# Kernel tuning notes

Hardware: AMD Instinct MI355X
Metric: run time of the kernel (lower is better)

The kernel has to match this reference:

```python
import jax, jax.numpy as jnp
from jax import lax
import numpy as np

B, C, H, W = 8, 256, 64, 64
DSTATE, DCONV, EXPAND = 16, 4, 2
DI = EXPAND * C          # 512 d_inner
DTR = (C + 15) // 16     # 16 dt_rank = ceil(d_model/16)

# ---------- helpers ----------

def _ln(x, g, b):
    m = x.mean(-1, keepdims=True)
    v = x.var(-1, keepdims=True)
    return (x - m) * lax.rsqrt(v + 1e-5) * g + b


def _bn(x, g, b):  # BatchNorm2d, training-mode batch stats
    m = x.mean((0, 2, 3), keepdims=True)
    v = x.var((0, 2, 3), keepdims=True)
    return (x - m) * lax.rsqrt(v + 1e-5) * g[None, :, None, None] + b[None, :, None, None]


def _gn(x, g, b, groups=32):
    Bb, Cc, Hh, Ww = x.shape
    xr = x.reshape(Bb, groups, Cc // groups, Hh, Ww)
    m = xr.mean((2, 3, 4), keepdims=True)
    v = xr.var((2, 3, 4), keepdims=True)
    xr = (xr - m) * lax.rsqrt(v + 1e-5)
    return xr.reshape(Bb, Cc, Hh, Ww) * g[None, :, None, None] + b[None, :, None, None]


def _hsig(x):  # h_sigmoid: relu6(x+3)/6
    return jnp.clip(x + 3.0, 0.0, 6.0) / 6.0


def _axial(v, idx, pos):
    # v: [B,C,N]; pos: [1,C,16] linearly resized to N (align_corners=False == half-pixel)
    N = v.shape[-1]
    pe = jax.image.resize(pos, (1, pos.shape[1], N), method='linear')
    return v + pe + idx  # idx interpolation is identity (same size)


def _dwconvT(x, w):
    # ConvTranspose2d(k=3, stride=2, pad=1, out_pad=1, groups=C) == lhs-dilated corr with flipped kernel
    wf = w[:, :, ::-1, ::-1]
    return lax.conv_general_dilated(x, wf, window_strides=(1, 1), padding=((1, 2), (1, 2)),
                                    lhs_dilation=(2, 2), dimension_numbers=('NCHW', 'OIHW', 'NCHW'),
                                    feature_group_count=x.shape[1])


def _mamba(h, in_w, conv_w, conv_b, xproj_w, dt_w, dt_b, Alog, Dp, out_w):
    # standard mamba_ssm Mamba block forward; h: [B,L,d_model]
    Bb, L, _ = h.shape
    di = in_w.shape[0] // 2
    N = Alog.shape[1]
    dtr = dt_w.shape[1]
    xz = h @ in_w.T                      # [B,L,2*di]
    xm, zg = xz[..., :di], xz[..., di:]
    # causal depthwise conv1d (pad K-1 left == torch pad both + slice [:L])
    xc = lax.conv_general_dilated(xm.transpose(0, 2, 1), conv_w, (1,), [(conv_w.shape[2] - 1, 0)],
                                  dimension_numbers=('NCH', 'OIH', 'NCH'), feature_group_count=di)
    u = jax.nn.silu(xc + conv_b[None, :, None]).transpose(0, 2, 1)  # [B,L,di]
    dbl = u @ xproj_w.T                  # [B,L,dtr+2N]
    dt = jax.nn.softplus(dbl[..., :dtr] @ dt_w.T + dt_b)            # [B,L,di]
    Bm = dbl[..., dtr:dtr + N]
    Cm = dbl[..., dtr + N:]
    A = -jnp.exp(Alog)                   # [di,N]
    dA = jnp.exp(dt[..., None] * A)      # [B,L,di,N]
    dBu = (dt * u)[..., None] * Bm[:, :, None, :]

    def step(hst, inp):
        dA_t, dBu_t = inp
        hst = dA_t * hst + dBu_t
        return hst, hst

    h0 = jnp.zeros((Bb, di, N), dt.dtype)
    _, hs = lax.scan(step, h0, (dA.transpose(1, 0, 2, 3), dBu.transpose(1, 0, 2, 3)))
    y = jnp.einsum('lbdn,bln->bld', hs, Cm) + Dp * u
    y = y * jax.nn.silu(zg)
    return y @ out_w.T


def _forward(x, pos_embed, ln_w, ln_b, proj_w, proj_b,
             up_dw_w, up_bn1_g, up_bn1_b, up_pw_w, up_bn2_g, up_bn2_b,
             down_pw_w, down_bn_g, down_bn_b, gn_g, gn_b,
             f_in_w, f_conv_w, f_conv_b, f_xproj_w, f_dt_w, f_dt_b, f_Alog, f_D, f_out_w,
             b_in_w, b_conv_w, b_conv_b, b_xproj_w, b_dt_w, b_dt_b, b_Alog, b_D, b_out_w):
    # upsample branch: dwconvT -> BN -> ReLU -> 1x1 -> BN -> ReLU6
    z = _dwconvT(x, up_dw_w)
    z = jax.nn.relu(_bn(z, up_bn1_g, up_bn1_b))
    z = jnp.einsum('oc,bchw->bohw', up_pw_w, z)
    z = jnp.clip(_bn(z, up_bn2_g, up_bn2_b), 0.0, 6.0)  # act1 = ReLU6
    dt = x.dtype
    col_max = _ln(_axial(x.max(2), jnp.argmax(x, 2).astype(dt), pos_embed).transpose(0, 2, 1), ln_w, ln_b)
    col_min = _ln(_axial(x.min(2), jnp.argmin(x, 2).astype(dt), pos_embed).transpose(0, 2, 1), ln_w, ln_b)
    row_max = _ln(_axial(x.max(3), jnp.argmax(x, 3).astype(dt), pos_embed).transpose(0, 2, 1), ln_w, ln_b)
    row_min = _ln(_axial(x.min(3), jnp.argmin(x, 3).astype(dt), pos_embed).transpose(0, 2, 1), ln_w, ln_b)
    result_max = jnp.concatenate([col_max, row_max], 1)  # [B, W+H, C]
    result_min = jnp.concatenate([col_min, row_min], 1)
    fpar = (f_in_w, f_conv_w, f_conv_b, f_xproj_w, f_dt_w, f_dt_b, f_Alog, f_D, f_out_w)
    bpar = (b_in_w, b_conv_w, b_conv_b, b_xproj_w, b_dt_w, b_dt_b, b_Alog, b_D, b_out_w)
    fmax = _ln(_mamba(result_max, *fpar), ln_w, ln_b)
    fmin = _ln(_mamba(result_min, *fpar), ln_w, ln_b)
    bmax = _ln(_mamba(jnp.flip(result_max, 1), *bpar), ln_w, ln_b)
    bmin = _ln(_mamba(jnp.flip(result_min, 1), *bpar), ln_w, ln_b)
    res_max = jnp.concatenate([fmax, jnp.flip(bmax, 1)], -1) @ proj_w.T + proj_b
    res_max = _ln(res_max, ln_w, ln_b)
    res_min = jnp.concatenate([fmin, jnp.flip(bmin, 1)], -1) @ proj_w.T + proj_b
    res_min = _ln(res_min, ln_w, ln_b)
    res = res_max[:, :, None, :] + res_min[:, None, :, :]  # [B,L,L,C], L=H+W
    res = res.transpose(0, 3, 1, 2)                        # [B,C,L,L] == [B,C,2H,2W]
    res = _hsig(res) * z
    res = _gn(res, gn_g, gn_b)
    res = jnp.einsum('oc,bchw->bohw', down_pw_w, res[:, :, ::2, ::2])  # 1x1 stride-2 conv
    res = _bn(res, down_bn_g, down_bn_b)
    res = _gn(res, gn_g, gn_b)
    res = res + x
    res = _gn(res, gn_g, gn_b)
    return res


def setup_inputs() -> dict:
    key = jax.random.key(0)
    ks = jax.random.split(key, 32)

    def n(i, shape, s=0.02):
        return jax.random.normal(ks[i], shape, jnp.float32) * s

    inp = {}
    inp['x'] = jax.random.normal(ks[0], (B, C, H, W), jnp.float32)
    inp['pos_embed'] = jax.random.normal(ks[1], (1, C, 16), jnp.float32)
    inp['ln_w'] = jnp.ones((C,), jnp.float32)
    inp['ln_b'] = jnp.zeros((C,), jnp.float32)
    inp['proj_w'] = n(2, (C, 2 * C))
    inp['proj_b'] = jnp.zeros((C,), jnp.float32)
    inp['up_dw_w'] = n(3, (C, 1, 3, 3), 0.1)
    inp['up_bn1_g'] = jnp.ones((C,), jnp.float32)
    inp['up_bn1_b'] = jnp.zeros((C,), jnp.float32)
    inp['up_pw_w'] = n(4, (C, C), 0.05)
    inp['up_bn2_g'] = jnp.ones((C,), jnp.float32)
    inp['up_bn2_b'] = jnp.zeros((C,), jnp.float32)
    inp['down_pw_w'] = n(5, (C, C), 0.05)
    inp['down_bn_g'] = jnp.ones((C,), jnp.float32)
    inp['down_bn_b'] = jnp.zeros((C,), jnp.float32)
    inp['gn_g'] = jnp.ones((C,), jnp.float32)
    inp['gn_b'] = jnp.zeros((C,), jnp.float32)
    Alog = jnp.tile(jnp.log(jnp.arange(1, DSTATE + 1, dtype=jnp.float32))[None, :], (DI, 1))
    dtb = jnp.full((DI,), float(np.log(np.expm1(0.01))), jnp.float32)
    for p, k0 in (('f', 6), ('b', 16)):
        inp[p + '_in_w'] = n(k0, (2 * DI, C))
        inp[p + '_conv_w'] = n(k0 + 1, (DI, 1, DCONV), 0.2)
        inp[p + '_conv_b'] = jnp.zeros((DI,), jnp.float32)
        inp[p + '_xproj_w'] = n(k0 + 2, (DTR + 2 * DSTATE, DI))
        inp[p + '_dt_w'] = n(k0 + 3, (DI, DTR), 0.1)
        inp[p + '_dt_b'] = dtb
        inp[p + '_Alog'] = Alog
        inp[p + '_D'] = jnp.ones((DI,), jnp.float32)
        inp[p + '_out_w'] = n(k0 + 4, (C, DI))
    return inp


def reference(x, pos_embed, ln_w, ln_b, proj_w, proj_b,
              up_dw_w, up_bn1_g, up_bn1_b, up_pw_w, up_bn2_g, up_bn2_b,
              down_pw_w, down_bn_g, down_bn_b, gn_g, gn_b,
              f_in_w, f_conv_w, f_conv_b, f_xproj_w, f_dt_w, f_dt_b, f_Alog, f_D, f_out_w,
              b_in_w, b_conv_w, b_conv_b, b_xproj_w, b_dt_w, b_dt_b, b_Alog, b_D, b_out_w):
    return _forward(x, pos_embed, ln_w, ln_b, proj_w, proj_b,
                    up_dw_w, up_bn1_g, up_bn1_b, up_pw_w, up_bn2_g, up_bn2_b,
                    down_pw_w, down_bn_g, down_bn_b, gn_g, gn_b,
                    f_in_w, f_conv_w, f_conv_b, f_xproj_w, f_dt_w, f_dt_b, f_Alog, f_D, f_out_w,
                    b_in_w, b_conv_w, b_conv_b, b_xproj_w, b_dt_w, b_dt_b, b_Alog, b_D, b_out_w)
```

## Files before the change

### kernel.cpp

```cpp
#include <hip/hip_runtime.h>
#include <hip/hip_bf16.h>

typedef __hip_bfloat16 bf16;
typedef __attribute__((ext_vector_type(8))) short bf16x8v;
typedef __attribute__((ext_vector_type(4))) short bf16x4v;
typedef __attribute__((ext_vector_type(4))) float f32x4v;

#define B_ 8
#define C_ 256
#define L_ 128
#define MB 1048576UL

__device__ inline float b2f(bf16 v){ return __bfloat162float(v); }
__device__ inline bf16 f2b(float v){ return __float2bfloat16(v); }
__device__ inline short b2s(bf16 v){ return *(short*)&v; }
__device__ inline float siluf(float x){ return x / (1.f + expf(-x)); }
__device__ inline float softplusf(float x){ return (x > 20.f) ? x : log1pf(expf(x)); }
__device__ inline float vclamp(float v){ return fmaxf(v, 0.f) + 1e-5f; }

__device__ inline void bred2(float& a, float& b, float* red){
  #pragma unroll
  for (int m = 1; m < 64; m <<= 1){ a += __shfl_xor(a, m); b += __shfl_xor(b, m); }
  int tid = threadIdx.x, wave = tid >> 6, lane = tid & 63;
  __syncthreads();
  if (lane == 0){ red[wave] = a; red[8 + wave] = b; }
  __syncthreads();
  a = red[0] + red[1] + red[2] + red[3];
  b = red[8] + red[9] + red[10] + red[11];
}

__device__ inline int tswz(int p, int c){
  return (p*512 + c*2) ^ (((p ^ (p >> 2)) & 7) << 4);
}

__global__ __launch_bounds__(64) void pool1_kernel(const float* __restrict__ x, const float* __restrict__ pos,
    float* __restrict__ pcolmax, float* __restrict__ pcolmin,
    float* __restrict__ prowmax, float* __restrict__ prowmin, float* __restrict__ sxb)
{
  int c = blockIdx.x, b = blockIdx.y, t = threadIdx.x;
  __shared__ float xs[64][65];
  const float* xp = x + ((long)(b*C_ + c))*4096;
  const float4* xp4 = (const float4*)xp;
  #pragma unroll
  for (int q = 0; q < 16; q++){
    float4 v = xp4[q*64 + t];
    int e = q*64 + t;
    int i = e >> 4, cc = (e & 15) << 2;
    xs[i][cc] = v.x; xs[i][cc+1] = v.y; xs[i][cc+2] = v.z; xs[i][cc+3] = v.w;
  }
  __syncthreads();
  float tt = 0.25f*(float)t - 0.375f;
  const float* pp = pos + c*16;
  float pe;
  if (tt <= 0.f) pe = pp[0];
  else if (tt >= 15.f) pe = pp[15];
  else { int f = (int)floorf(tt); float w = tt - (float)f; pe = pp[f]*(1.f - w) + pp[f+1]*w; }
  float vmax = -1e30f, vmin = 1e30f; int amax = 0, amin = 0;
  for (int j = 0; j < 64; j++){
    float v = xs[t][j];
    if (v > vmax){ vmax = v; amax = j; }
    if (v < vmin){ vmin = v; amin = j; }
  }
  long o = (long)(b*64 + t)*C_ + c;
  prowmax[o] = vmax + pe + (float)amax;
  prowmin[o] = vmin + pe + (float)amin;
  vmax = -1e30f; vmin = 1e30f; amax = 0; amin = 0;
  float sx = 0.f, sx2 = 0.f;
  for (int i = 0; i < 64; i++){
    float v = xs[i][t];
    if (v > vmax){ vmax = v; amax = i; }
    if (v < vmin){ vmin = v; amin = i; }
    sx += v; sx2 += v*v;
  }
  pcolmax[o] = vmax + pe + (float)amax;
  pcolmin[o] = vmin + pe + (float)amin;
  #pragma unroll
  for (int m = 1; m < 64; m <<= 1){ sx += __shfl_xor(sx, m); sx2 += __shfl_xor(sx2, m); }
  if (t == 0){ sxb[(b << 8) + c] = sx; sxb[2048 + (b << 8) + c] = sx2; }
}

__global__ __launch_bounds__(256) void pool2_kernel(const float* __restrict__ pcolmax, const float* __restrict__ pcolmin,
    const float* __restrict__ prowmax, const float* __restrict__ prowmin,
    const float* __restrict__ lnw, const float* __restrict__ lnb, bf16* __restrict__ hbuf)
{
  int r = blockIdx.x, b = blockIdx.y, c = threadIdx.x;
  __shared__ float red[16];
  int p = r & 63;
  long src = (long)(b*64 + p)*C_ + c;
  float vmax = (r < 64) ? pcolmax[src] : prowmax[src];
  float vmin = (r < 64) ? pcolmin[src] : prowmin[src];
  float gw = lnw[c], gb = lnb[c];
  long row = (long)b*L_ + r, frow = (long)b*L_ + (127 - r);
  float s = vmax, s2 = vmax*vmax;
  bred2(s, s2, red);
  float m = s*(1.f/256.f), var = s2*(1.f/256.f) - m*m;
  float o = (vmax - m)*rsqrtf(vclamp(var))*gw + gb;
  hbuf[0*262144 + row*C_ + c]  = f2b(o);
  hbuf[2*262144 + frow*C_ + c] = f2b(o);
  s = vmin; s2 = vmin*vmin;
  bred2(s, s2, red);
  m = s*(1.f/256.f); var = s2*(1.f/256.f) - m*m;
  o = (vmin - m)*rsqrtf(vclamp(var))*gw + gb;
  hbuf[1*262144 + row*C_ + c]  = f2b(o);
  hbuf[3*262144 + frow*C_ + c] = f2b(o);
}

__global__ __launch_bounds__(256) void dwz1_kernel(const float* __restrict__ x, const float* __restrict__ dw,
    bf16* __restrict__ z1, float* __restrict__ bn1sum, float* __restrict__ bn1sq)
{
  int bc = blockIdx.x; int c = bc & 255;
  int tid = threadIdx.x;
  __shared__ __align__(16) float xs[4096];
  const float4* xp4 = (const float4*)(x + (long)bc*4096);
  #pragma unroll
  for (int q = 0; q < 4; q++)
    *(float4*)&xs[(q*256 + tid)*4] = xp4[q*256 + tid];
  float w[9];
  #pragma unroll
  for (int q = 0; q < 9; q++) w[q] = dw[c*9 + q];
  __syncthreads();
  bf16* zp = z1 + (long)bc*16384;
  float s = 0.f, s2 = 0.f;
  for (int it = 0; it < 64; it++){
    int p = it*256 + tid; int i = p >> 7, j = p & 127;
    int xi = i >> 1, xj = j >> 1;
    int io = i & 1, jo = j & 1;
    int xi1 = (xi < 63) ? xi + 1 : 63;
    int xj1 = (xj < 63) ? xj + 1 : 63;
    float XA = xs[xi*64 + xj];
    float XB = xs[xi*64 + xj1];
    float XC = xs[xi1*64 + xj];
    float XD = xs[xi1*64 + xj1];
    float wA = jo ? (io ? w[8] : w[5]) : (io ? w[7] : w[4]);
    float wB = (jo && j < 127) ? (io ? w[6] : w[3]) : 0.f;
    float wC = (io && i < 127) ? (jo ? w[2] : w[1]) : 0.f;
    float wD = (io && jo && i < 127 && j < 127) ? w[0] : 0.f;
    float acc = wA*XA;
    acc += wB*XB;
    acc += wC*XC;
    acc += wD*XD;
    zp[p] = f2b(acc);
    s += acc; s2 += acc*acc;
  }
  __shared__ float red[16];
  bred2(s, s2, red);
  if (tid == 0){ atomicAdd(&bn1sum[c], s); atomicAdd(&bn1sq[c], s2); }
}

__global__ __launch_bounds__(256) void wcvt_all_kernel(
    const float* __restrict__ s0, const float* __restrict__ s1, const float* __restrict__ s2,
    const float* __restrict__ s3, const float* __restrict__ s4, const float* __restrict__ s5,
    const float* __restrict__ s6, const float* __restrict__ s7, const float* __restrict__ s8,
    bf16* __restrict__ d0, bf16* __restrict__ d1, bf16* __restrict__ d2,
    bf16* __restrict__ d3, bf16* __restrict__ d4, bf16* __restrict__ d5,
    bf16* __restrict__ d6, bf16* __restrict__ d7, bf16* __restrict__ d8)
{
  int seg = blockIdx.y;
  const float* s; bf16* d; int n;
  switch (seg){
    case 0: s = s0; d = d0; n = 262144; break;
    case 1: s = s1; d = d1; n = 262144; break;
    case 2: s = s2; d = d2; n = 24576;  break;
    case 3: s = s3; d = d3; n = 24576;  break;
    case 4: s = s4; d = d4; n = 131072; break;
    case 5: s = s5; d = d5; n = 131072; break;
    case 6: s = s6; d = d6; n = 131072; break;
    case 7: s = s7; d = d7; n = 65536;  break;
    default: s = s8; d = d8; n = 65536; break;
  }
  long i = ((long)blockIdx.x*256 + threadIdx.x)*4;
  if (i >= n) return;
  float4 v = *(const float4*)&s[i];
  bf16 o[4] = {f2b(v.x), f2b(v.y), f2b(v.z), f2b(v.w)};
  *(uint2*)&d[i] = *(const uint2*)o;
}

__global__ __launch_bounds__(256) void pwz_fused_kernel(const bf16* __restrict__ z1,
    const float* __restrict__ bn1sum, const float* __restrict__ bn1sq,
    const float* __restrict__ g1, const float* __restrict__ b1,
    const bf16* __restrict__ Wb, bf16* __restrict__ z2,
    float* __restrict__ bn2part)
{
  int b = blockIdx.y;
  int p0 = blockIdx.x*64;
  int tid = threadIdx.x;
  __shared__ __align__(16) short Tb[16384];
  __shared__ float aa[256], dd[256];
  {
    float m = bn1sum[tid]*(1.f/131072.f);
    float v = bn1sq[tid]*(1.f/131072.f) - m*m;
    float a = g1[tid]*rsqrtf(vclamp(v));
    aa[tid] = a; dd[tid] = b1[tid] - m*a;
  }
  __syncthreads();
  {
    int pc = tid & 15, ch = tid >> 4;
    #pragma unroll
    for (int it = 0; it < 8; it++){
      int c = (ch + it*16)*2;
      const bf16* r0 = &z1[((long)(b*C_ + c))*16384 + p0 + pc*4];
      bf16x4v va = *(const bf16x4v*)r0;
      bf16x4v vb = *(const bf16x4v*)(r0 + 16384);
      float a0 = aa[c], d0 = dd[c], a1 = aa[c+1], d1 = dd[c+1];
      #pragma unroll
      for (int k = 0; k < 4; k++){
        int p = pc*4 + k;
        bf16 h0; *(short*)&h0 = va[k];
        bf16 h1; *(short*)&h1 = vb[k];
        bf16 o0 = f2b(fmaxf(b2f(h0)*a0 + d0, 0.f));
        bf16 o1 = f2b(fmaxf(b2f(h1)*a1 + d1, 0.f));
        unsigned int u = ((unsigned int)(*(unsigned short*)&o1) << 16) | (unsigned int)(*(unsigned short*)&o0);
        *(unsigned int*)((char*)Tb + tswz(p, c)) = u;
      }
    }
  }
  __syncthreads();
  int wave = tid >> 6, lane = tid & 63;
  int quad = lane >> 4, l16 = lane & 15;
  f32x4v acc[4][4];
  #pragma unroll
  for (int i = 0; i < 4; i++)
    #pragma unroll
    for (int j = 0; j < 4; j++) acc[i][j] = (f32x4v){0.f, 0.f, 0.f, 0.f};
  for (int k0 = 0; k0 < 256; k0 += 32){
    int c = k0 + quad*8;
    bf16x8v a[4], bb[4];
    #pragma unroll
    for (int ms = 0; ms < 4; ms++)
      a[ms] = *(const bf16x8v*)&Wb[(wave*64 + ms*16 + l16)*C_ + c];
    #pragma unroll
    for (int ns = 0; ns < 4; ns++){
      int p = ns*16 + l16;
      bb[ns] = *(const bf16x8v*)((const char*)Tb + tswz(p, c));
    }
    #pragma unroll
    for (int ms = 0; ms < 4; ms++)
      #pragma unroll
      for (int ns = 0; ns < 4; ns++)
        acc[ms][ns] = __builtin_amdgcn_mfma_f32_16x16x32_bf16(bb[ns], a[ms], acc[ms][ns], 0, 0, 0);
  }
  int slot = (blockIdx.x & 7) | (b << 3);
  #pragma unroll
  for (int ms = 0; ms < 4; ms++){
    int o = wave*64 + ms*16 + l16;
    long rowbase = ((long)(b*C_ + o))*16384 + p0;
    float s = 0.f, s2 = 0.f;
    #pragma unroll
    for (int ns = 0; ns < 4; ns++){
      bf16 ov[4];
      #pragma unroll
      for (int r = 0; r < 4; r++){
        bf16 bv = f2b(acc[ms][ns][r]);
        ov[r] = bv;
        float vv = b2f(bv);
        s += vv; s2 += vv*vv;
      }
      *(uint2*)&z2[rowbase + ns*16 + quad*4] = *(const uint2*)ov;
    }
    s += __shfl_xor(s, 16);  s += __shfl_xor(s, 32);
    s2 += __shfl_xor(s2, 16); s2 += __shfl_xor(s2, 32);
    if (quad == 0){
      atomicAdd(&bn2part[slot*256 + o], s);
      atomicAdd(&bn2part[16384 + slot*256 + o], s2);
    }
  }
}

__global__ __launch_bounds__(256) void inproj_mfma_kernel(const bf16* __restrict__ hb,
    const bf16* __restrict__ Wif, const bf16* __restrict__ Wib2, bf16* __restrict__ xz)
{
  int v = blockIdx.z;
  int m0 = blockIdx.y*256, n0 = blockIdx.x*64;
  const bf16* A = hb + (long)v*262144;
  const bf16* W = (v >= 2) ? Wib2 : Wif;
  bf16* out = xz + (long)v*1048576;
  int tid = threadIdx.x;
  int wave = tid >> 6, lane = tid & 63;
  int quad = lane >> 4, l16 = lane & 15;
  f32x4v acc[4][4];
  #pragma unroll
  for (int i = 0; i < 4; i++)
    #pragma unroll
    for (int j = 0; j < 4; j++) acc[i][j] = (f32x4v){0.f, 0.f, 0.f, 0.f};
  for (int k0 = 0; k0 < 256; k0 += 32){
    int c = k0 + quad*8;
    bf16x8v a[4], bb[4];
    #pragma unroll
    for (int ms = 0; ms < 4; ms++)
      a[ms] = *(const bf16x8v*)&A[(long)(m0 + wave*64 + ms*16 + l16)*256 + c];
    #pragma unroll
    for (int ns = 0; ns < 4; ns++)
      bb[ns] = *(const bf16x8v*)&W[(long)(n0 + ns*16 + l16)*256 + c];
    #pragma unroll
    for (int ms = 0; ms < 4; ms++)
      #pragma unroll
      for (int ns = 0; ns < 4; ns++)
        acc[ms][ns] = __builtin_amdgcn_mfma_f32_16x16x32_bf16(bb[ns], a[ms], acc[ms][ns], 0, 0, 0);
  }
  #pragma unroll
  for (int ms = 0; ms < 4; ms++){
    int m = m0 + wave*64 + ms*16 + l16;
    #pragma unroll
    for (int ns = 0; ns < 4; ns++){
      bf16 ov[4];
      #pragma unroll
      for (int r = 0; r < 4; r++) ov[r] = f2b(acc[ms][ns][r]);
      *(uint2*)&out[(long)m*1024 + n0 + ns*16 + quad*4] = *(const uint2*)ov;
    }
  }
}

__global__ __launch_bounds__(256) void xproj_mfma_kernel(const bf16* __restrict__ ub,
    const bf16* __restrict__ Wxf, const bf16* __restrict__ Wxb, float* __restrict__ dblb)
{
  int v = blockIdx.y;
  int m0 = blockIdx.x*256;
  const bf16* A = ub + (long)v*524288;
  const bf16* W = (v >= 2) ? Wxb : Wxf;
  float* out = dblb + (long)v*49152;
  int tid = threadIdx.x;
  int wave = tid >> 6, lane = tid & 63;
  int quad = lane >> 4, l16 = lane & 15;
  f32x4v acc[4][3];
  #pragma unroll
  for (int i = 0; i < 4; i++)
    #pragma unroll
    for (int j = 0; j < 3; j++) acc[i][j] = (f32x4v){0.f, 0.f, 0.f, 0.f};
  for (int k0 = 0; k0 < 512; k0 += 32){
    int c = k0 + quad*8;
    bf16x8v a[4], bb[3];
    #pragma unroll
    for (int ms = 0; ms < 4; ms++)
      a[ms] = *(const bf16x8v*)&A[(long)(m0 + wave*64 + ms*16 + l16)*512 + c];
    #pragma unroll
    for (int ns = 0; ns < 3; ns++)
      bb[ns] = *(const bf16x8v*)&W[(long)(ns*16 + l16)*512 + c];
    #pragma unroll
    for (int ms = 0; ms < 4; ms++)
      #pragma unroll
      for (int ns = 0; ns < 3; ns++)
        acc[ms][ns] = __builtin_amdgcn_mfma_f32_16x16x32_bf16(bb[ns], a[ms], acc[ms][ns], 0, 0, 0);
  }
  #pragma unroll
  for (int ms = 0; ms < 4; ms++){
    int m = m0 + wave*64 + ms*16 + l16;
    #pragma unroll
    for (int ns = 0; ns < 3; ns++)
      *(f32x4v*)&out[(long)m*48 + ns*16 + quad*4] = acc[ms][ns];
  }
}

__global__ __launch_bounds__(256) void outproj_mfma_kernel(const bf16* __restrict__ yb,
    const bf16* __restrict__ Wof, const bf16* __restrict__ Wob, float* __restrict__ mo)
{
  int v = blockIdx.z;
  int m0 = blockIdx.y*256, n0 = blockIdx.x*64;
  const bf16* A = yb + (long)v*524288;
  const bf16* W = (v >= 2) ? Wob : Wof;
  float* out = mo + (long)v*262144;
  int tid = threadIdx.x;
  int wave = tid >> 6, lane = tid & 63;
  int quad = lane >> 4, l16 = lane & 15;
  f32x4v acc[4][4];
  #pragma unroll
  for (int i = 0; i < 4; i++)
    #pragma unroll
    for (int j = 0; j < 4; j++) acc[i][j] = (f32x4v){0.f, 0.f, 0.f, 0.f};
  for (int k0 = 0; k0 < 512; k0 += 32){
    int c = k0 + quad*8;
    bf16x8v a[4], bb[4];
    #pragma unroll
    for (int ms = 0; ms < 4; ms++)
      a[ms] = *(const bf16x8v*)&A[(long)(m0 + wave*64 + ms*16 + l16)*512 + c];
    #pragma unroll
    for (int ns = 0; ns < 4; ns++)
      bb[ns] = *(const bf16x8v*)&W[(long)(n0 + ns*16 + l16)*512 + c];
    #pragma unroll
    for (int ms = 0; ms < 4; ms++)
      #pragma unroll
      for (int ns = 0; ns < 4; ns++)
        acc[ms][ns] = __builtin_amdgcn_mfma_f32_16x16x32_bf16(bb[ns], a[ms], acc[ms][ns], 0, 0, 0);
  }
  #pragma unroll
  for (int ms = 0; ms < 4; ms++){
    int m = m0 + wave*64 + ms*16 + l16;
    #pragma unroll
    for (int ns = 0; ns < 4; ns++)
      *(f32x4v*)&out[(long)m*256 + n0 + ns*16 + quad*4] = acc[ms][ns];
  }
}

__global__ __launch_bounds__(256) void pj_mfma_kernel(const bf16* __restrict__ cb,
    const bf16* __restrict__ Wp, const float* __restrict__ pb, float* __restrict__ rp)
{
  int z = blockIdx.z;
  int m0 = blockIdx.y*256, n0 = blockIdx.x*64;
  const bf16* A = cb + (long)z*524288;
  float* out = rp + (long)z*262144;
  int tid = threadIdx.x;
  int wave = tid >> 6, lane = tid & 63;
  int quad = lane >> 4, l16 = lane & 15;
  f32x4v acc[4][4];
  #pragma unroll
  for (int i = 0; i < 4; i++)
    #pragma unroll
    for (int j = 0; j < 4; j++) acc[i][j] = (f32x4v){0.f, 0.f, 0.f, 0.f};
  for (int k0 = 0; k0 < 512; k0 += 32){
    int c = k0 + quad*8;
    bf16x8v a[4], bb[4];
    #pragma unroll
    for (int ms = 0; ms < 4; ms++)
      a[ms] = *(const bf16x8v*)&A[(long)(m0 + wave*64 + ms*16 + l16)*512 + c];
    #pragma unroll
    for (int ns = 0; ns < 4; ns++)
      bb[ns] = *(const bf16x8v*)&Wp[(long)(n0 + ns*16 + l16)*512 + c];
    #pragma unroll
    for (int ms = 0; ms < 4; ms++)
      #pragma unroll
      for (int ns = 0; ns < 4; ns++)
        acc[ms][ns] = __builtin_amdgcn_mfma_f32_16x16x32_bf16(bb[ns], a[ms], acc[ms][ns], 0, 0, 0);
  }
  #pragma unroll
  for (int ns = 0; ns < 4; ns++){
    float4 pbv = *(const float4*)&pb[n0 + ns*16 + quad*4];
    #pragma unroll
    for (int ms = 0; ms < 4; ms++){
      int m = m0 + wave*64 + ms*16 + l16;
      f32x4v vv = acc[ms][ns];
      vv[0] += pbv.x; vv[1] += pbv.y; vv[2] += pbv.z; vv[3] += pbv.w;
      *(f32x4v*)&out[(long)m*256 + n0 + ns*16 + quad*4] = vv;
    }
  }
}

__global__ __launch_bounds__(256) void gemm_kernel(
  const float* __restrict__ Abase, long sA, int lda,
  const float* __restrict__ W0, const float* __restrict__ W1,
  const float* __restrict__ bias0, const float* __restrict__ bias1, int wsplit,
  float* __restrict__ Cbase, long sC, int ldc,
  int M, int N, int K, int act)
{
  int z = blockIdx.z;
  const float* A = Abase + (long)z*sA;
  const float* W = (z >= wsplit) ? W1 : W0;
  const float* bias = (z >= wsplit) ? bias1 : bias0;
  int m0 = blockIdx.y*64, n0 = blockIdx.x*64;
  __shared__ __align__(16) float As[16][68];
  __shared__ __align__(16) float Ws[16][68];
  int tid = threadIdx.x, tx = tid & 15, ty = tid >> 4;
  float acc[4][4] = {};
  for (int k0 = 0; k0 < K; k0 += 16){
    #pragma unroll
    for (int q = 0; q < 4; q++){
      int e = tid + q*256; int r = e >> 4, kk = e & 15;
      int mi = m0 + r, ki = k0 + kk;
      As[kk][r] = (mi < M && ki < K) ? A[(long)mi*lda + ki] : 0.f;
    }
    #pragma unroll
    for (int q = 0; q < 4; q++){
      int e = tid + q*256; int n = e >> 4, kk = e & 15;
      int ni = n0 + n, ki = k0 + kk;
      Ws[kk][n] = (ni < N && ki < K) ? W[(long)ni*K + ki] : 0.f;
    }
    __syncthreads();
    #pragma unroll
    for (int kk = 0; kk < 16; kk++){
      float4 a4 = *(const float4*)&As[kk][ty*4];
      float4 b4 = *(const float4*)&Ws[kk][tx*4];
      float av[4] = {a4.x, a4.y, a4.z, a4.w};
      float bv[4] = {b4.x, b4.y, b4.z, b4.w};
      #pragma unroll
      for (int mm = 0; mm < 4; mm++)
        #pragma unroll
        for (int nn = 0; nn < 4; nn++) acc[mm][nn] += av[mm]*bv[nn];
    }
    __syncthreads();
  }
  #pragma unroll
  for (int mm = 0; mm < 4; mm++){
    int mi = m0 + ty*4 + mm;
    if (mi >= M) continue;
    #pragma unroll
    for (int nn = 0; nn < 4; nn++){
      int ni = n0 + tx*4 + nn;
      if (ni >= N) continue;
      float v = acc[mm][nn];
      if (bias) v += bias[ni];
      if (act >= 2) v = softplusf(v);
      if (act == 3){
        bf16* Cb = (bf16*)Cbase + (long)z*sC;
        Cb[(long)mi*ldc + ni] = f2b(v);
      } else {
        float* Cp = Cbase + (long)z*sC;
        Cp[(long)mi*ldc + ni] = v;
      }
    }
  }
}

__global__ __launch_bounds__(512) void conv1d_kernel(const bf16* __restrict__ xzb,
    const float* __restrict__ fw, const float* __restrict__ fb,
    const float* __restrict__ bw, const float* __restrict__ bb,
    bf16* __restrict__ ub)
{
  int l = blockIdx.x, b = blockIdx.y, v = blockIdx.z, d = threadIdx.x;
  const bf16* xm = xzb + (long)v*1024*1024;
  const float* w  = (v < 2) ? fw : bw;
  const float* cb = (v < 2) ? fb : bb;
  float acc = cb[d];
  #pragma unroll
  for (int k = 0; k < 4; k++){
    int ll = l - 3 + k;
    if (ll >= 0) acc += b2f(xm[(long)(b*L_ + ll)*1024 + d]) * w[d*4 + k];
  }
  ub[(long)v*1024*512 + (long)(b*L_ + l)*512 + d] = f2b(siluf(acc));
}

__global__ __launch_bounds__(64) void scan_kernel(const bf16* __restrict__ dtb, const bf16* __restrict__ ub,
    const float* __restrict__ dblb, const bf16* __restrict__ xzb,
    const float* __restrict__ fAlog, const float* __restrict__ fD,
    const float* __restrict__ bAlog, const float* __restrict__ bD,
    bf16* __restrict__ yb)
{
  int v = blockIdx.z, b = blockIdx.y;
  int tid = threadIdx.x;
  int dd = tid & 15, qtr = tid >> 4;
  int d0 = blockIdx.x*16;
  int d = d0 + dd;
  const bf16*  dt  = dtb  + (long)v*1024*512;
  const bf16*  u   = ub   + (long)v*1024*512;
  const float* dbl = dblb + (long)v*1024*48;
  const bf16*  zg  = xzb  + (long)v*1024*1024 + 512;
  const float* Alog = (v < 2) ? fAlog : bAlog;
  const float* Dp   = (v < 2) ? fD : bD;
  __shared__ __align__(16) short sdt[16][136];
  __shared__ __align__(16) short su_[16][136];
  __shared__ __align__(16) short szg[16][136];
  __shared__ __align__(16) short sB [16][136];
  __shared__ __align__(16) short sC [16][136];
  long row = (long)b*L_;
  for (int idx = tid; idx < 2048; idx += 64){
    int l = idx >> 4, j = idx & 15;
    sdt[j][l] = b2s(dt[(row + l)*512 + d0 + j]);
    su_[j][l] = b2s(u[(row + l)*512 + d0 + j]);
    szg[j][l] = b2s(zg[(row + l)*1024 + d0 + j]);
    sB [j][l] = b2s(f2b(dbl[(row + l)*48 + 16 + j]));
    sC [j][l] = b2s(f2b(dbl[(row + l)*48 + 32 + j]));
  }
  float a2[4];
  #pragma unroll
  for (int n = 0; n < 4; n++) a2[n] = -expf(Alog[d*16 + qtr*4 + n]) * 1.44269504f;
  float Dv = Dp[d];
  float h[4];
  #pragma unroll
  for (int n = 0; n < 4; n++) h[n] = 0.f;
  __syncthreads();
  bf16* yo = yb + (long)v*1024*512;
  for (int l0 = 0; l0 < 128; l0 += 8){
    bf16x8v dt8 = *(const bf16x8v*)&sdt[dd][l0];
    bf16x8v u8  = *(const bf16x8v*)&su_[dd][l0];
    bf16x8v zg8 = *(const bf16x8v*)&szg[dd][l0];
    bf16x8v B8[4], C8[4];
    #pragma unroll
    for (int n = 0; n < 4; n++){
      B8[n] = *(const bf16x8v*)&sB[qtr*4 + n][l0];
      C8[n] = *(const bf16x8v*)&sC[qtr*4 + n][l0];
    }
    #pragma unroll
    for (int k = 0; k < 8; k++){
      bf16 t0; *(short*)&t0 = dt8[k]; float dtv = b2f(t0);
      bf16 t1; *(short*)&t1 = u8[k];  float uv  = b2f(t1);
      bf16 t2; *(short*)&t2 = zg8[k]; float zgv = b2f(t2);
      float dtu = dtv*uv;
      float acc = 0.f;
      #pragma unroll
      for (int n = 0; n < 4; n++){
        float dA = exp2f(dtv*a2[n]);
        bf16 tb; *(short*)&tb = B8[n][k];
        bf16 tc; *(short*)&tc = C8[n][k];
        h[n] = dA*h[n] + dtu*b2f(tb);
        acc += h[n]*b2f(tc);
      }
      acc += __shfl_xor(acc, 16);
      acc += __shfl_xor(acc, 32);
      if (qtr == 0)
        yo[(row + l0 + k)*512 + d] = f2b((acc + Dv*uv) * siluf(zgv));
    }
  }
}

__global__ __launch_bounds__(256) void ln_kernel(const float* __restrict__ inb, bf16* __restrict__ outb0,
    bf16* __restrict__ outb1, float* __restrict__ outf,
    const float* __restrict__ lnw, const float* __restrict__ lnb, int mode)
{
  int r = blockIdx.x, b = blockIdx.y, v = blockIdx.z, c = threadIdx.x;
  long row = (long)b*L_ + r;
  float val = inb[((long)v*1024 + row)*C_ + c];
  __shared__ float red[16];
  float s = val, s2 = val*val;
  bred2(s, s2, red);
  float m = s*(1.f/256.f), var = s2*(1.f/256.f) - m*m;
  float o = (val - m)*rsqrtf(vclamp(var))*lnw[c] + lnb[c];
  if (mode == 1){
    long frow = (long)b*L_ + (127 - r);
    if (v == 0)      outb0[row*512 + c] = f2b(o);
    else if (v == 1) outb1[row*512 + c] = f2b(o);
    else if (v == 2) outb0[frow*512 + 256 + c] = f2b(o);
    else             outb1[frow*512 + 256 + c] = f2b(o);
  } else {
    outf[((long)v*1024 + row)*C_ + c] = o;
  }
}

__global__ __launch_bounds__(256) void hsig_kernel(bf16* __restrict__ z2, const float* __restrict__ rm,
    const float* __restrict__ rn, const float* __restrict__ bn2part,
    const float* __restrict__ g2, const float* __restrict__ b2,
    float* __restrict__ gnsum, float* __restrict__ gnsq)
{
  int c = blockIdx.x, b = blockIdx.y, tid = threadIdx.x;
  __shared__ float red[16];
  __shared__ float rms[128], rns[128];
  if (tid < 128){
    rms[tid] = rm[(long)(b*L_ + tid)*C_ + c];
    rns[tid] = rn[(long)(b*L_ + tid)*C_ + c];
  }
  float pa = 0.f, pb = 0.f;
  if (tid < 64){ pa = bn2part[tid*256 + c]; pb = bn2part[16384 + tid*256 + c]; }
  bred2(pa, pb, red);
  float mm2 = pa*(1.f/131072.f);
  float vv2 = pb*(1.f/131072.f) - mm2*mm2;
  float aa = g2[c] * rsqrtf(vclamp(vv2));
  float dd = b2[c] - mm2*aa;
  bf16* zp = z2 + ((long)(b*C_ + c))*16384;
  float pre[16];
  #pragma unroll
  for (int g = 0; g < 4; g++)
    #pragma unroll
    for (int q = 0; q < 4; q++)
      pre[g*4 + q] = b2f(zp[g*1024 + q*256 + tid]);
  __syncthreads();
  float s = 0.f, s2 = 0.f;
  #pragma unroll
  for (int g = 0; g < 4; g++){
    #pragma unroll
    for (int q = 0; q < 4; q++){
      int p = g*1024 + q*256 + tid; int i = p >> 7, j = p & 127;
      float zv = pre[g*4 + q]*aa + dd;
      zv = fminf(fmaxf(zv, 0.f), 6.f);
      float gate = rms[i] + rns[j];
      gate = fminf(fmaxf(gate + 3.f, 0.f), 6.f) * (1.f/6.f);
      float t = gate*zv;
      s += t; s2 += t*t;
      if (((i | j) & 1) == 0) zp[(i >> 1)*64 + (j >> 1)] = f2b(t);
    }
  }
  for (int g = 4; g < 16; g++){
    #pragma unroll
    for (int q = 0; q < 4; q++){
      int p = g*1024 + q*256 + tid; int i = p >> 7, j = p & 127;
      float zv = b2f(zp[p])*aa + dd;
      zv = fminf(fmaxf(zv, 0.f), 6.f);
      float gate = rms[i] + rns[j];
      gate = fminf(fmaxf(gate + 3.f, 0.f), 6.f) * (1.f/6.f);
      float t = gate*zv;
      s += t; s2 += t*t;
      if (((i | j) & 1) == 0) zp[(i >> 1)*64 + (j >> 1)] = f2b(t);
    }
  }
  bred2(s, s2, red);
  if (tid == 0){ atomicAdd(&gnsum[b*32 + (c >> 3)], s); atomicAdd(&gnsq[b*32 + (c >> 3)], s2); }
}

__global__ __launch_bounds__(256) void pwdown_fused_kernel(const bf16* __restrict__ z2,
    const float* __restrict__ gnsum, const float* __restrict__ gnsq,
    const float* __restrict__ gn_g, const float* __restrict__ gn_b,
    const bf16* __restrict__ Wb, const float* __restrict__ x,
    float* __restrict__ out, float* __restrict__ sds)
{
  int b = blockIdx.y;
  int p0 = blockIdx.x*64;
  int tid = threadIdx.x;
  __shared__ __align__(16) short Tb[16384];
  __shared__ float gA[256], gD[256];
  {
    float m = gnsum[b*32 + (tid >> 3)]*(1.f/131072.f);
    float v = gnsq[b*32 + (tid >> 3)]*(1.f/131072.f) - m*m;
    float A = rsqrtf(vclamp(v))*gn_g[tid];
    gA[tid] = A; gD[tid] = gn_b[tid] - m*A;
  }
  __syncthreads();
  {
    int pc = tid & 15, ch = tid >> 4;
    #pragma unroll
    for (int it = 0; it < 8; it++){
      int c = (ch + it*16)*2;
      const bf16* r0 = &z2[((long)(b*C_ + c))*16384 + p0 + pc*4];
      bf16x4v va = *(const bf16x4v*)r0;
      bf16x4v vb = *(const bf16x4v*)(r0 + 16384);
      float a0 = gA[c], d0 = gD[c];
      float a1 = gA[c + 1], d1 = gD[c + 1];
      #pragma unroll
      for (int k = 0; k < 4; k++){
        int p = pc*4 + k;
        bf16 h0; *(short*)&h0 = va[k];
        bf16 h1; *(short*)&h1 = vb[k];
        bf16 o0 = f2b(b2f(h0)*a0 + d0);
        bf16 o1 = f2b(b2f(h1)*a1 + d1);
        unsigned int u = ((unsigned int)(*(unsigned short*)&o1) << 16) | (unsigned int)(*(unsigned short*)&o0);
        *(unsigned int*)((char*)Tb + tswz(p, c)) = u;
      }
    }
  }
  __syncthreads();
  int wave = tid >> 6, lane = tid & 63;
  int quad = lane >> 4, l16 = lane & 15;
  f32x4v acc[4][4];
  #pragma unroll
  for (int i = 0; i < 4; i++)
    #pragma unroll
    for (int j = 0; j < 4; j++) acc[i][j] = (f32x4v){0.f, 0.f, 0.f, 0.f};
  for (int k0 = 0; k0 < 256; k0 += 32){
    int c = k0 + quad*8;
    bf16x8v a[4], bb[4];
    #pragma unroll
    for (int ms = 0; ms < 4; ms++)
      a[ms] = *(const bf16x8v*)&Wb[(wave*64 + ms*16 + l16)*C_ + c];
    #pragma unroll
    for (int ns = 0; ns < 4; ns++){
      int p = ns*16 + l16;
      bb[ns] = *(const bf16x8v*)((const char*)Tb + tswz(p, c));
    }
    #pragma unroll
    for (int ms = 0; ms < 4; ms++)
      #pragma unroll
      for (int ns = 0; ns < 4; ns++)
        acc[ms][ns] = __builtin_amdgcn_mfma_f32_16x16x32_bf16(bb[ns], a[ms], acc[ms][ns], 0, 0, 0);
  }
  #pragma unroll
  for (int ms = 0; ms < 4; ms++){
    int o = wave*64 + ms*16 + l16;
    long rowbase = ((long)(b*C_ + o))*4096 + p0;
    float sd = 0.f, sd2 = 0.f, sdx = 0.f;
    #pragma unroll
    for (int ns = 0; ns < 4; ns++){
      f32x4v v4 = acc[ms][ns];
      long base = rowbase + ns*16 + quad*4;
      *(f32x4v*)&out[base] = v4;
      float4 xv = *(const float4*)&x[base];
      sd += v4[0] + v4[1] + v4[2] + v4[3];
      sd2 += v4[0]*v4[0] + v4[1]*v4[1] + v4[2]*v4[2] + v4[3]*v4[3];
      sdx += v4[0]*xv.x + v4[1]*xv.y + v4[2]*xv.z + v4[3]*xv.w;
    }
    sd += __shfl_xor(sd, 16);  sd += __shfl_xor(sd, 32);
    sd2 += __shfl_xor(sd2, 16); sd2 += __shfl_xor(sd2, 32);
    sdx += __shfl_xor(sdx, 16); sdx += __shfl_xor(sdx, 32);
    if (quad == 0){
      int oc = (b << 8) + o;
      atomicAdd(&sds[oc], sd);
      atomicAdd(&sds[2048 + oc], sd2);
      atomicAdd(&sds[4096 + oc], sdx);
    }
  }
}

__global__ __launch_bounds__(256) void final_kernel(const float* __restrict__ x,
    const float* __restrict__ sds, const float* __restrict__ sxb,
    const float* __restrict__ dbn_g, const float* __restrict__ dbn_b,
    const float* __restrict__ gn_g, const float* __restrict__ gn_b,
    float* __restrict__ out)
{
  int c = blockIdx.x, b = blockIdx.y, tid = threadIdx.x;
  __shared__ float lv[11][8];
  int g8 = (c >> 3) << 3;
  if (tid < 8){
    int cc = g8 + tid;
    float sd = 0.f, sd2 = 0.f;
    for (int bb2 = 0; bb2 < 8; bb2++){ sd += sds[bb2*256 + cc]; sd2 += sds[2048 + bb2*256 + cc]; }
    float mB = sd*(1.f/32768.f);
    float vB = sd2*(1.f/32768.f) - mB*mB;
    float ab = dbn_g[cc] * rsqrtf(vclamp(vB));
    float db = dbn_b[cc] - mB*ab;
    float inv_n = 1.f/4096.f;
    float m = sds[b*256 + cc]*inv_n, Ed2 = sds[2048 + b*256 + cc]*inv_n;
    float mx = sxb[b*256 + cc]*inv_n, Ex2 = sxb[2048 + b*256 + cc]*inv_n;
    float Edx = sds[4096 + b*256 + cc]*inv_n;
    float Ev = ab*m + db;
    float Ev2 = ab*ab*Ed2 + 2.f*ab*db*m + db*db;
    lv[0][tid] = ab; lv[1][tid] = db; lv[2][tid] = m; lv[3][tid] = Ed2;
    lv[4][tid] = mx; lv[5][tid] = Ex2; lv[6][tid] = Edx; lv[7][tid] = Ev; lv[8][tid] = Ev2;
  }
  __syncthreads();
  if (tid < 8){
    float m1 = 0.f, q1 = 0.f;
    for (int k = 0; k < 8; k++){ m1 += lv[7][k]; q1 += lv[8][k]; }
    m1 *= 0.125f; q1 *= 0.125f;
    int cc = g8 + tid;
    float inv1 = rsqrtf(vclamp(q1 - m1*m1));
    float A1 = inv1*gn_g[cc];
    float D1 = gn_b[cc] - m1*A1;
    float ab = lv[0][tid], db = lv[1][tid];
    float m = lv[2][tid], Ed2 = lv[3][tid], mx = lv[4][tid], Ex2 = lv[5][tid], Edx = lv[6][tid];
    float al = A1*ab;
    float be = A1*db + D1;
    float Et = al*m + be + mx;
    float Et2 = al*al*Ed2 + 2.f*al*be*m + be*be + 2.f*al*Edx + 2.f*be*mx + Ex2;
    lv[9][tid] = Et; lv[10][tid] = Et2; lv[0][tid] = al; lv[1][tid] = be;
  }
  __syncthreads();
  float m2 = 0.f, q2 = 0.f;
  for (int k = 0; k < 8; k++){ m2 += lv[9][k]; q2 += lv[10][k]; }
  m2 *= 0.125f; q2 *= 0.125f;
  float G = rsqrtf(vclamp(q2 - m2*m2))*gn_g[c];
  float P = G*lv[0][c & 7];
  float Q = G;
  float R = G*(lv[1][c & 7] - m2) + gn_b[c];
  long base = ((long)(b*C_ + c))*1024;
  const float4* x4 = (const float4*)x;
  float4* o4 = (float4*)out;
  #pragma unroll
  for (int it = 0; it < 4; it++){
    long idx = base + it*256 + tid;
    float4 o = o4[idx];
    float4 xv = x4[idx];
    o.x = P*o.x + Q*xv.x + R;
    o.y = P*o.y + Q*xv.y + R;
    o.z = P*o.z + Q*xv.z + R;
    o.w = P*o.w + Q*xv.w + R;
    o4[idx] = o;
  }
}

extern "C" void kernel_launch(void* const* d_in, const int* in_sizes, int n_in,
                              void* d_out, int out_size, void* d_ws, size_t ws_size,
                              hipStream_t stream)
{
  (void)in_sizes; (void)n_in; (void)out_size; (void)ws_size;
  const float* x         = (const float*)d_in[0];
  const float* pos       = (const float*)d_in[1];
  const float* ln_w      = (const float*)d_in[2];
  const float* ln_b      = (const float*)d_in[3];
  const float* proj_w    = (const float*)d_in[4];
  const float* proj_b    = (const float*)d_in[5];
  const float* up_dw_w   = (const float*)d_in[6];
  const float* up_bn1_g  = (const float*)d_in[7];
  const float* up_bn1_b  = (const float*)d_in[8];
  const float* up_pw_w   = (const float*)d_in[9];
  const float* up_bn2_g  = (const float*)d_in[10];
  const float* up_bn2_b  = (const float*)d_in[11];
  const float* down_pw_w = (const float*)d_in[12];
  const float* down_bn_g = (const float*)d_in[13];
  const float* down_bn_b = (const float*)d_in[14];
  const float* gn_g      = (const float*)d_in[15];
  const float* gn_b      = (const float*)d_in[16];
  const float* f_in_w    = (const float*)d_in[17];
  const float* f_conv_w  = (const float*)d_in[18];
  const float* f_conv_b  = (const float*)d_in[19];
  const float* f_xproj_w = (const float*)d_in[20];
  const float* f_dt_w    = (const float*)d_in[21];
  const float* f_dt_b    = (const float*)d_in[22];
  const float* f_Alog    = (const float*)d_in[23];
  const float* f_D       = (const float*)d_in[24];
  const float* f_out_w   = (const float*)d_in[25];
  const float* b_in_w    = (const float*)d_in[26];
  const float* b_conv_w  = (const float*)d_in[27];
  const float* b_conv_b  = (const float*)d_in[28];
  const float* b_xproj_w = (const float*)d_in[29];
  const float* b_dt_w    = (const float*)d_in[30];
  const float* b_dt_b    = (const float*)d_in[31];
  const float* b_Alog    = (const float*)d_in[32];
  const float* b_D       = (const float*)d_in[33];
  const float* b_out_w   = (const float*)d_in[34];

  char* sb = (char*)d_ws;
  float* statz  = (float*)(sb);
  float* sds    = (float*)(sb + 6144);
  float* bn2part= (float*)(sb + 32768);
  float* sxb    = (float*)(sb + 184320);
  float* rmrn  = (float*)(sb + 1*MB);
  bf16*  Wbbuf = (bf16*)(sb + 3*MB);
  bf16*  Wb2buf= (bf16*)(sb + 3*MB + 262144);
  bf16*  Wpb   = (bf16*)(sb + 3*MB + 524288);
  char* big = sb + 4*MB;
  float* pool4  = (float*)(big + 0*MB);
  bf16*  hbufb  = (bf16*)(big + 2*MB);
  bf16*  Wif    = (bf16*)(big + 4*MB);
  bf16*  Wib2   = (bf16*)(big + 4*MB + 524288);
  bf16*  Wxf    = (bf16*)(big + 5*MB);
  bf16*  Wxb    = (bf16*)(big + 5*MB + 65536);
  bf16*  Wof    = (bf16*)(big + 5*MB + 131072);
  bf16*  Wob    = (bf16*)(big + 5*MB + 393216);
  bf16*  xzbuf  = (bf16*)(big + 6*MB);
  bf16*  ubuf   = (bf16*)(big + 22*MB);
  float* dblbuf = (float*)(big + 30*MB);
  bf16*  dtbuf  = (bf16*)(big + 31*MB);
  bf16*  ybuf   = (bf16*)(big + 39*MB);
  float* mout   = (float*)(big + 47*MB);
  bf16*  cbufb  = (bf16*)(big + 51*MB);
  float* respre = (float*)(big + 55*MB);
  bf16*  z1buf  = (bf16*)(big);
  bf16*  z2buf  = (bf16*)(big);
  float* dbuf   = (float*)d_out;

  float* bn1sum = statz;        float* bn1sq = statz + 256;
  float* gnsum  = statz + 1024; float* gnsq  = statz + 1280;
  float* pcolmax = pool4;
  float* pcolmin = pool4 + 131072;
  float* prowmax = pool4 + 262144;
  float* prowmin = pool4 + 393216;

  hipMemsetAsync(statz, 0, 163840, stream);

  wcvt_all_kernel<<<dim3(256, 9), 256, 0, stream>>>(
      f_in_w, b_in_w, f_xproj_w, b_xproj_w, f_out_w, b_out_w, proj_w, up_pw_w, down_pw_w,
      Wif, Wib2, Wxf, Wxb, Wof, Wob, Wpb, Wbbuf, Wb2buf);

  pool1_kernel<<<dim3(256, 8), 64, 0, stream>>>(x, pos, pcolmax, pcolmin, prowmax, prowmin, sxb);
  pool2_kernel<<<dim3(128, 8), 256, 0, stream>>>(pcolmax, pcolmin, prowmax, prowmin, ln_w, ln_b, hbufb);
  inproj_mfma_kernel<<<dim3(16, 4, 4), 256, 0, stream>>>(hbufb, Wif, Wib2, xzbuf);
  conv1d_kernel<<<dim3(128, 8, 4), 512, 0, stream>>>(xzbuf, f_conv_w, f_conv_b, b_conv_w, b_conv_b, ubuf);
  xproj_mfma_kernel<<<dim3(4, 4), 256, 0, stream>>>(ubuf, Wxf, Wxb, dblbuf);
  gemm_kernel<<<dim3(8, 16, 4), 256, 0, stream>>>(dblbuf, 49152, 48, f_dt_w, b_dt_w, f_dt_b, b_dt_b, 2,
                                                  (float*)dtbuf, 524288, 512, 1024, 512, 16, 3);
  scan_kernel<<<dim3(32, 8, 4), 64, 0, stream>>>(dtbuf, ubuf, dblbuf, xzbuf, f_Alog, f_D, b_Alog, b_D, ybuf);
  outproj_mfma_kernel<<<dim3(4, 4, 4), 256, 0, stream>>>(ybuf, Wof, Wob, mout);
  ln_kernel<<<dim3(128, 8, 4), 256, 0, stream>>>(mout, cbufb, cbufb + 524288, nullptr, ln_w, ln_b, 1);
  pj_mfma_kernel<<<dim3(4, 4, 2), 256, 0, stream>>>(cbufb, Wpb, proj_b, respre);
  ln_kernel<<<dim3(128, 8, 2), 256, 0, stream>>>(respre, nullptr, nullptr, rmrn, ln_w, ln_b, 0);

  dwz1_kernel<<<2048, 256, 0, stream>>>(x, up_dw_w, z1buf, bn1sum, bn1sq);
  pwz_fused_kernel<<<dim3(256, 8), 256, 0, stream>>>(z1buf, bn1sum, bn1sq, up_bn1_g, up_bn1_b,
                                                     Wbbuf, z2buf, bn2part);

  hsig_kernel<<<dim3(256, 8), 256, 0, stream>>>(z2buf, rmrn, rmrn + 262144, bn2part,
                                                up_bn2_g, up_bn2_b, gnsum, gnsq);
  pwdown_fused_kernel<<<dim3(64, 8), 256, 0, stream>>>(z2buf, gnsum, gnsq, gn_g, gn_b,
                                                       Wb2buf, x, dbuf, sds);
  final_kernel<<<dim3(256, 8), 256, 0, stream>>>(x, sds, sxb, down_bn_g, down_bn_b, gn_g, gn_b,
                                                 (float*)d_out);
}
```

Before: 486.7 us.

## Restructure dwconvT, hsig, and scan kernels for vectorized access and more parallelism

The transposed depthwise conv now computes the 2x2 output quad per input pixel and writes paired bf16 values, which removes per-output branching and quarters the shared-memory reads. The hsig kernel now reads 8 bf16 values per thread with vector loads and writes the downsampled output as packed 64-bit stores instead of scattered scalar accesses. The scan kernel handles 8 channels per block with 2 states per thread, doubling the grid to expose more parallelism, at the cost of an extra shuffle reduction and B/C staged redundantly in more blocks.

```diff
diff --git a/kernel.cpp b/kernel.cpp
--- a/kernel.cpp
+++ b/kernel.cpp
@@ -121,26 +121,32 @@
   __syncthreads();
   bf16* zp = z1 + (long)bc*16384;
   float s = 0.f, s2 = 0.f;
-  for (int it = 0; it < 64; it++){
-    int p = it*256 + tid; int i = p >> 7, j = p & 127;
-    int xi = i >> 1, xj = j >> 1;
-    int io = i & 1, jo = j & 1;
-    int xi1 = (xi < 63) ? xi + 1 : 63;
-    int xj1 = (xj < 63) ? xj + 1 : 63;
-    float XA = xs[xi*64 + xj];
-    float XB = xs[xi*64 + xj1];
-    float XC = xs[xi1*64 + xj];
-    float XD = xs[xi1*64 + xj1];
-    float wA = jo ? (io ? w[8] : w[5]) : (io ? w[7] : w[4]);
-    float wB = (jo && j < 127) ? (io ? w[6] : w[3]) : 0.f;
-    float wC = (io && i < 127) ? (jo ? w[2] : w[1]) : 0.f;
-    float wD = (io && jo && i < 127 && j < 127) ? w[0] : 0.f;
-    float acc = wA*XA;
-    acc += wB*XB;
-    acc += wC*XC;
-    acc += wD*XD;
-    zp[p] = f2b(acc);
-    s += acc; s2 += acc*acc;
+  for (int it = 0; it < 16; it++){
+    int q = it*256 + tid;
+    int a = q >> 6, bq = q & 63;
+    int a1 = (a < 63) ? a + 1 : 63;
+    int b1 = (bq < 63) ? bq + 1 : 63;
+    float XA = xs[a*64 + bq];
+    float XB = xs[a*64 + b1];
+    float XC = xs[a1*64 + bq];
+    float XD = xs[a1*64 + b1];
+    float w3e = (bq < 63) ? w[3] : 0.f;
+    float w6e = (bq < 63) ? w[6] : 0.f;
+    float w1e = (a < 63) ? w[1] : 0.f;
+    float w2e = (a < 63) ? w[2] : 0.f;
+    float w0e = (a < 63 && bq < 63) ? w[0] : 0.f;
+    float o00 = w[4]*XA; o00 += 0.f*XB; o00 += 0.f*XC; o00 += 0.f*XD;
+    float o01 = w[5]*XA; o01 += w3e*XB; o01 += 0.f*XC; o01 += 0.f*XD;
+    float o10 = w[7]*XA; o10 += 0.f*XB; o10 += w1e*XC; o10 += 0.f*XD;
+    float o11 = w[8]*XA; o11 += w6e*XB; o11 += w2e*XC; o11 += w0e*XD;
+    bf16 r0[2] = {f2b(o00), f2b(o01)};
+    bf16 r1[2] = {f2b(o10), f2b(o11)};
+    *(unsigned int*)&zp[(2*a)*128 + 2*bq]     = *(const unsigned int*)r0;
+    *(unsigned int*)&zp[(2*a + 1)*128 + 2*bq] = *(const unsigned int*)r1;
+    s += o00; s2 += o00*o00;
+    s += o01; s2 += o01*o01;
+    s += o10; s2 += o10*o10;
+    s += o11; s2 += o11*o11;
   }
   __shared__ float red[16];
   bred2(s, s2, red);
@@ -524,8 +530,8 @@
 {
   int v = blockIdx.z, b = blockIdx.y;
   int tid = threadIdx.x;
-  int dd = tid & 15, qtr = tid >> 4;
-  int d0 = blockIdx.x*16;
+  int dd = tid & 7, qtr = tid >> 3;
+  int d0 = blockIdx.x*8;
   int d = d0 + dd;
   const bf16*  dt  = dtb  + (long)v*1024*512;
   const bf16*  u   = ub   + (long)v*1024*512;
@@ -533,38 +539,40 @@
   const bf16*  zg  = xzb  + (long)v*1024*1024 + 512;
   const float* Alog = (v < 2) ? fAlog : bAlog;
   const float* Dp   = (v < 2) ? fD : bD;
-  __shared__ __align__(16) short sdt[16][136];
-  __shared__ __align__(16) short su_[16][136];
-  __shared__ __align__(16) short szg[16][136];
+  __shared__ __align__(16) short sdt[8][136];
+  __shared__ __align__(16) short su_[8][136];
+  __shared__ __align__(16) short szg[8][136];
   __shared__ __align__(16) short sB [16][136];
   __shared__ __align__(16) short sC [16][136];
   long row = (long)b*L_;
-  for (int idx = tid; idx < 2048; idx += 64){
-    int l = idx >> 4, j = idx & 15;
+  for (int idx = tid; idx < 1024; idx += 64){
+    int l = idx >> 3, j = idx & 7;
     sdt[j][l] = b2s(dt[(row + l)*512 + d0 + j]);
     su_[j][l] = b2s(u[(row + l)*512 + d0 + j]);
     szg[j][l] = b2s(zg[(row + l)*1024 + d0 + j]);
-    sB [j][l] = b2s(f2b(dbl[(row + l)*48 + 16 + j]));
-    sC [j][l] = b2s(f2b(dbl[(row + l)*48 + 32 + j]));
-  }
-  float a2[4];
-  #pragma unroll
-  for (int n = 0; n < 4; n++) a2[n] = -expf(Alog[d*16 + qtr*4 + n]) * 1.44269504f;
+  }
+  for (int idx = tid; idx < 2048; idx += 64){
+    int l = idx >> 4, j = idx & 15;
+    sB[j][l] = b2s(f2b(dbl[(row + l)*48 + 16 + j]));
+    sC[j][l] = b2s(f2b(dbl[(row + l)*48 + 32 + j]));
+  }
+  float a2[2];
+  #pragma unroll
+  for (int n = 0; n < 2; n++) a2[n] = -expf(Alog[d*16 + qtr*2 + n]) * 1.44269504f;
   float Dv = Dp[d];
-  float h[4];
-  #pragma unroll
-  for (int n = 0; n < 4; n++) h[n] = 0.f;
+  float h[2];
+  h[0] = 0.f; h[1] = 0.f;
   __syncthreads();
   bf16* yo = yb + (long)v*1024*512;
   for (int l0 = 0; l0 < 128; l0 += 8){
     bf16x8v dt8 = *(const bf16x8v*)&sdt[dd][l0];
     bf16x8v u8  = *(const bf16x8v*)&su_[dd][l0];
     bf16x8v zg8 = *(const bf16x8v*)&szg[dd][l0];
-    bf16x8v B8[4], C8[4];
-    #pragma unroll
-    for (int n = 0; n < 4; n++){
-      B8[n] = *(const bf16x8v*)&sB[qtr*4 + n][l0];
-      C8[n] = *(const bf16x8v*)&sC[qtr*4 + n][l0];
+    bf16x8v B8[2], C8[2];
+    #pragma unroll
+    for (int n = 0; n < 2; n++){
+      B8[n] = *(const bf16x8v*)&sB[qtr*2 + n][l0];
+      C8[n] = *(const bf16x8v*)&sC[qtr*2 + n][l0];
     }
     #pragma unroll
     for (int k = 0; k < 8; k++){
@@ -574,13 +582,14 @@
       float dtu = dtv*uv;
       float acc = 0.f;
       #pragma unroll
-      for (int n = 0; n < 4; n++){
+      for (int n = 0; n < 2; n++){
         float dA = exp2f(dtv*a2[n]);
         bf16 tb; *(short*)&tb = B8[n][k];
         bf16 tc; *(short*)&tc = C8[n][k];
         h[n] = dA*h[n] + dtu*b2f(tb);
         acc += h[n]*b2f(tc);
       }
+      acc += __shfl_xor(acc, 8);
       acc += __shfl_xor(acc, 16);
       acc += __shfl_xor(acc, 32);
       if (qtr == 0)
@@ -632,40 +641,33 @@
   float aa = g2[c] * rsqrtf(vclamp(vv2));
   float dd = b2[c] - mm2*aa;
   bf16* zp = z2 + ((long)(b*C_ + c))*16384;
-  float pre[16];
-  #pragma unroll
-  for (int g = 0; g < 4; g++)
-    #pragma unroll
-    for (int q = 0; q < 4; q++)
-      pre[g*4 + q] = b2f(zp[g*1024 + q*256 + tid]);
+  int j0 = (tid & 15)*8;
+  int irow = tid >> 4;
+  bf16x8v pre0 = *(const bf16x8v*)&zp[0*2048 + tid*8];
+  bf16x8v pre1 = *(const bf16x8v*)&zp[1*2048 + tid*8];
   __syncthreads();
   float s = 0.f, s2 = 0.f;
   #pragma unroll
-  for (int g = 0; g < 4; g++){
-    #pragma unroll
-    for (int q = 0; q < 4; q++){
-      int p = g*1024 + q*256 + tid; int i = p >> 7, j = p & 127;
-      float zv = pre[g*4 + q]*aa + dd;
+  for (int g = 0; g < 8; g++){
+    bf16x8v v8;
+    if (g == 0) v8 = pre0;
+    else if (g == 1) v8 = pre1;
+    else v8 = *(const bf16x8v*)&zp[g*2048 + tid*8];
+    int i = g*16 + irow;
+    bf16 ov[4];
+    #pragma unroll
+    for (int k = 0; k < 8; k++){
+      bf16 t; *(short*)&t = v8[k];
+      float zv = b2f(t)*aa + dd;
       zv = fminf(fmaxf(zv, 0.f), 6.f);
-      float gate = rms[i] + rns[j];
+      float gate = rms[i] + rns[j0 + k];
       gate = fminf(fmaxf(gate + 3.f, 0.f), 6.f) * (1.f/6.f);
-      float t = gate*zv;
-      s += t; s2 += t*t;
-      if (((i | j) & 1) == 0) zp[(i >> 1)*64 + (j >> 1)] = f2b(t);
-    }
-  }
-  for (int g = 4; g < 16; g++){
-    #pragma unroll
-    for (int q = 0; q < 4; q++){
-      int p = g*1024 + q*256 + tid; int i = p >> 7, j = p & 127;
-      float zv = b2f(zp[p])*aa + dd;
-      zv = fminf(fmaxf(zv, 0.f), 6.f);
-      float gate = rms[i] + rns[j];
-      gate = fminf(fmaxf(gate + 3.f, 0.f), 6.f) * (1.f/6.f);
-      float t = gate*zv;
-      s += t; s2 += t*t;
-      if (((i | j) & 1) == 0) zp[(i >> 1)*64 + (j >> 1)] = f2b(t);
-    }
+      float t2 = gate*zv;
+      s += t2; s2 += t2*t2;
+      if ((k & 1) == 0) ov[k >> 1] = f2b(t2);
+    }
+    if ((i & 1) == 0)
+      *(uint2*)&zp[(i >> 1)*64 + (tid & 15)*4] = *(const uint2*)ov;
   }
   bred2(s, s2, red);
   if (tid == 0){ atomicAdd(&gnsum[b*32 + (c >> 3)], s); atomicAdd(&gnsq[b*32 + (c >> 3)], s2); }
@@ -921,7 +923,7 @@
   xproj_mfma_kernel<<<dim3(4, 4), 256, 0, stream>>>(ubuf, Wxf, Wxb, dblbuf);
   gemm_kernel<<<dim3(8, 16, 4), 256, 0, stream>>>(dblbuf, 49152, 48, f_dt_w, b_dt_w, f_dt_b, b_dt_b, 2,
                                                   (float*)dtbuf, 524288, 512, 1024, 512, 16, 3);
-  scan_kernel<<<dim3(32, 8, 4), 64, 0, stream>>>(dtbuf, ubuf, dblbuf, xzbuf, f_Alog, f_D, b_Alog, b_D, ybuf);
+  scan_kernel<<<dim3(64, 8, 4), 64, 0, stream>>>(dtbuf, ubuf, dblbuf, xzbuf, f_Alog, f_D, b_Alog, b_D, ybuf);
   outproj_mfma_kernel<<<dim3(4, 4, 4), 256, 0, stream>>>(ybuf, Wof, Wob, mout);
   ln_kernel<<<dim3(128, 8, 4), 256, 0, stream>>>(mout, cbufb, cbufb + 524288, nullptr, ln_w, ln_b, 1);
   pj_mfma_kernel<<<dim3(4, 4, 2), 256, 0, stream>>>(cbufb, Wpb, proj_b, respre);
```

Result: faster. 468.4 us (-3.8%).
